# Performance work log

Hardware: AMD Instinct MI355X
Metric: run time of the kernel (lower is better)

## Reference

```python
import jax, jax.numpy as jnp
import numpy as np

NUM_HEADS = 16

def setup_inputs() -> dict:
    key = jax.random.key(0)
    k1, k2, k3 = jax.random.split(key, 3)
    B, N, C = 4, 4096, 1024
    x = jax.random.normal(k1, (B, N, C), dtype=jnp.float32)
    # xavier-uniform-ish scaled init for the dense kernels
    w_qkv = jax.random.normal(k2, (C, 3 * C), dtype=jnp.float32) * (2.0 / (C + 3 * C)) ** 0.5
    w_proj = jax.random.normal(k3, (C, C), dtype=jnp.float32) * (1.0 / C) ** 0.5
    b_proj = jnp.zeros((C,), dtype=jnp.float32)
    return {"x": x, "w_qkv": w_qkv, "w_proj": w_proj, "b_proj": b_proj}

def reference(x, w_qkv, w_proj, b_proj):
    B, N, C = x.shape
    H = NUM_HEADS
    D = C // H
    # qkv projection: (B, N, 3C) -> (3, B, H, N, D)
    qkv = (x @ w_qkv).reshape(B, N, 3, H, D).transpose(2, 0, 3, 1, 4)
    q, k, v = qkv[0], qkv[1], qkv[2]
    # feature map: elu + 1 (positive features)
    q = jax.nn.elu(q) + 1.0
    k = jax.nn.elu(k) + 1.0
    # kv outer-product accumulation: (B, H, D, D)
    kv = jnp.einsum('bhnd,bhne->bhde', k, v)
    numerator = jnp.einsum('bhnd,bhde->bhne', q, kv)        # (B, H, N, D)
    sum_k = k.sum(axis=-2)                                   # (B, H, D)
    denominator = jnp.einsum('bhnd,bhd->bhn', q, sum_k)[..., None]  # (B, H, N, 1)
    y = numerator / denominator                              # (B, H, N, D)
    y = y.transpose(0, 2, 1, 3).reshape(B, N, C)             # merge heads
    out = y @ w_proj + b_proj
    return out
```

## Files before the change

### kernel.cpp

```cpp
#include <hip/hip_runtime.h>

typedef __bf16 bf16x8 __attribute__((ext_vector_type(8)));
typedef float f32x4 __attribute__((ext_vector_type(4)));

typedef const unsigned int __attribute__((address_space(1)))* gas_p;
typedef unsigned int __attribute__((address_space(3)))* las_p;

__device__ __forceinline__ void gload_lds16(const void* g, void* l) {
  __builtin_amdgcn_global_load_lds((gas_p)g, (las_p)l, 16, 0, 0);
}

__device__ __forceinline__ unsigned short f2bf(float f) {
  union { float f; unsigned int u; } x; x.f = f;
  unsigned int r = x.u + 0x7fffu + ((x.u >> 16) & 1u);
  return (unsigned short)(r >> 16);
}
__device__ __forceinline__ float elu1(float x) {
  return x > 0.f ? x + 1.f : __expf(x);
}
__device__ __forceinline__ f32x4 mfma16(bf16x8 a, bf16x8 b, f32x4 c) {
  return __builtin_amdgcn_mfma_f32_16x16x32_bf16(a, b, c, 0, 0, 0);
}

#define BAR() __builtin_amdgcn_s_barrier()
#define VMW0() asm volatile("s_waitcnt vmcnt(0)" ::: "memory")


__global__ __launch_bounds__(256) void k_cvt_x(const float* __restrict__ x,
                                               unsigned short* __restrict__ xb, int n) {
  int i = (blockIdx.x * 256 + threadIdx.x) * 4;
  const int stride = gridDim.x * 256 * 4;
  for (; i < n; i += stride) {
    float4 v = *(const float4*)(x + i);
    union { unsigned short u[4]; uint2 q; } pk;
    pk.u[0] = f2bf(v.x); pk.u[1] = f2bf(v.y); pk.u[2] = f2bf(v.z); pk.u[3] = f2bf(v.w);
    *(uint2*)(xb + i) = pk.q;
  }
}

__global__ __launch_bounds__(256) void k_cvt_t(const float* __restrict__ w,
                                               unsigned short* __restrict__ wT,
                                               int R, int Cc) {
  __shared__ float t[32][33];
  const int j0 = blockIdx.x * 32, i0 = blockIdx.y * 32;
  const int tx = threadIdx.x & 31, ty = threadIdx.x >> 5;
#pragma unroll
  for (int k = 0; k < 4; ++k)
    t[ty + 8 * k][tx] = w[(size_t)(i0 + ty + 8 * k) * Cc + j0 + tx];
  __syncthreads();
#pragma unroll
  for (int k = 0; k < 4; ++k)
    wT[(size_t)(j0 + ty + 8 * k) * R + i0 + tx] = f2bf(t[tx][ty + 8 * k]);
}


template <int EPI>
__global__ __launch_bounds__(512, 2) void k_gemm256(
    const unsigned short* __restrict__ A, const unsigned short* __restrict__ BT, int NBX,
    unsigned short* __restrict__ qb, unsigned short* __restrict__ kT,
    unsigned short* __restrict__ vT, const float* __restrict__ bias,
    float* __restrict__ out) {
  extern __shared__ unsigned short lds[];
  unsigned short* Asb = lds;
  unsigned short* Bsb = lds + 32768;

  const int tid = threadIdx.x, lane = tid & 63, wave = tid >> 6;
  const int wm = wave >> 2, wn = wave & 3;
  int bid = blockIdx.x;
  { const int cpx = (int)gridDim.x >> 3; bid = (bid & 7) * cpx + (bid >> 3); }
  const int bx = bid % NBX, by = bid / NBX;
  const size_t bm0 = (size_t)by << 8, bn0 = (size_t)bx << 8;

  const int srow = (wave << 4) + (lane >> 2);
  const int gscol = ((lane & 3) << 3) ^ (((srow >> 1) & 3) << 3);
  const unsigned short* Ag0 = A + (bm0 + srow) * 1024 + gscol;
  const unsigned short* Bg0 = BT + (bn0 + srow) * 1024 + gscol;
  const int lws = wave << 9;

  auto stageA = [&](int pair) {
    const unsigned short* g_ = Ag0 + (pair << 5);
    unsigned short* l_ = Asb + ((pair & 3) << 13) + lws;
    gload_lds16(g_, l_);
    gload_lds16(g_ + 128 * 1024, l_ + 4096);
  };
  auto stageB = [&](int pair) {
    const unsigned short* g_ = Bg0 + (pair << 5);
    unsigned short* l_ = Bsb + ((pair & 3) << 13) + lws;
    gload_lds16(g_, l_);
    gload_lds16(g_ + 128 * 1024, l_ + 4096);
  };

  const int q8 = ((lane >> 4) << 3) ^ (((lane >> 1) & 3) << 3);
  const int ar_base = (wm << 7) + (lane & 15);
  const int br_base = (wn << 6) + (lane & 15);

  f32x4 acc[8][4] = {};

  stageA(0); stageB(0); stageA(1); stageB(1);
  VMW0();
  BAR();

#pragma unroll
  for (int t = 0; t < 16; ++t) {
    const int o0 = ((2 * t) & 3) << 13, o1 = ((2 * t + 1) & 3) << 13;

    if (t < 15) { stageA(2 * t + 2); stageB(2 * t + 2); stageA(2 * t + 3); stageB(2 * t + 3); }

    bf16x8 a0[4], a1[4], b0[4], b1[4];
#pragma unroll
    for (int mi = 0; mi < 4; ++mi)
      a0[mi] = *(const bf16x8*)&Asb[o0 + ((ar_base + mi * 16) << 5) + q8];
#pragma unroll
    for (int n = 0; n < 4; ++n)
      b0[n] = *(const bf16x8*)&Bsb[o0 + ((br_base + n * 16) << 5) + q8];
#pragma unroll
    for (int mi = 0; mi < 4; ++mi)
      a1[mi] = *(const bf16x8*)&Asb[o1 + ((ar_base + mi * 16) << 5) + q8];
#pragma unroll
    for (int n = 0; n < 4; ++n)
      b1[n] = *(const bf16x8*)&Bsb[o1 + ((br_base + n * 16) << 5) + q8];
    __builtin_amdgcn_s_setprio(1);
#pragma unroll
    for (int mi = 0; mi < 4; ++mi)
#pragma unroll
      for (int n = 0; n < 4; ++n) acc[mi][n] = mfma16(a0[mi], b0[n], acc[mi][n]);
#pragma unroll
    for (int mi = 0; mi < 4; ++mi)
#pragma unroll
      for (int n = 0; n < 4; ++n) acc[mi][n] = mfma16(a1[mi], b1[n], acc[mi][n]);
    __builtin_amdgcn_s_setprio(0);

#pragma unroll
    for (int mi = 0; mi < 4; ++mi)
      a0[mi] = *(const bf16x8*)&Asb[o0 + ((ar_base + 64 + mi * 16) << 5) + q8];
#pragma unroll
    for (int mi = 0; mi < 4; ++mi)
      a1[mi] = *(const bf16x8*)&Asb[o1 + ((ar_base + 64 + mi * 16) << 5) + q8];
    __builtin_amdgcn_s_setprio(1);
#pragma unroll
    for (int mi = 0; mi < 4; ++mi)
#pragma unroll
      for (int n = 0; n < 4; ++n) acc[4 + mi][n] = mfma16(a0[mi], b0[n], acc[4 + mi][n]);
#pragma unroll
    for (int mi = 0; mi < 4; ++mi)
#pragma unroll
      for (int n = 0; n < 4; ++n) acc[4 + mi][n] = mfma16(a1[mi], b1[n], acc[4 + mi][n]);
    __builtin_amdgcn_s_setprio(0);

    if (t < 15) VMW0();
    BAR();
  }

  const int rbase = (int)bm0 + (wm << 7) + ((lane >> 4) << 2);
  const int cbase = (int)bn0 + (wn << 6) + (lane & 15);
  if constexpr (EPI == 0) {
    const int reg3 = (int)(bn0 >> 10);
#pragma unroll
    for (int m = 0; m < 8; ++m) {
      const int rb = rbase + m * 16;
#pragma unroll
      for (int n = 0; n < 4; ++n) {
        const int col = cbase + n * 16;
        if (reg3 == 0) {
#pragma unroll
          for (int i = 0; i < 4; ++i)
            qb[(size_t)(rb + i) * 1024 + col] = f2bf(elu1(acc[m][n][i]));
        } else {
          const int jc = col & 1023, h = jc >> 6, d = jc & 63;
          const int b_ = rb >> 12, n_ = rb & 4095;
          union { unsigned short u[4]; uint2 q; } pk;
          if (reg3 == 1) {
#pragma unroll
            for (int i = 0; i < 4; ++i) pk.u[i] = f2bf(elu1(acc[m][n][i]));
          } else {
#pragma unroll
            for (int i = 0; i < 4; ++i) pk.u[i] = f2bf(acc[m][n][i]);
          }
          unsigned short* dst = (reg3 == 1) ? kT : vT;
          *(uint2*)(dst + ((size_t)((b_ * 16 + h) * 64 + d) * 4096 + n_)) = pk.q;
        }
      }
    }
  } else {
#pragma unroll
    for (int n = 0; n < 4; ++n) {
      const int col = cbase + n * 16;
      const float bc = bias[col];
#pragma unroll
      for (int m = 0; m < 8; ++m) {
        const int rb = rbase + m * 16;
#pragma unroll
        for (int i = 0; i < 4; ++i)
          out[(size_t)(rb + i) * 1024 + col] = acc[m][n][i] + bc;
      }
    }
  }
}


__global__ __launch_bounds__(256) void k_kvpart(const unsigned short* __restrict__ kT,
                                                const unsigned short* __restrict__ vT,
                                                float* __restrict__ kvp,
                                                float* __restrict__ sumkp) {
  __shared__ unsigned short Ks[64 * 64];
  __shared__ unsigned short Vs[64 * 64];
  const int blk = blockIdx.x;
  const int bh = blk >> 3, ch = blk & 7;
  const int tid = threadIdx.x, lane = tid & 63, wave = tid >> 6;
  const unsigned short* kb = kT + (size_t)bh * 64 * 4096;
  const unsigned short* vb = vT + (size_t)bh * 64 * 4096;
  const int n0 = ch * 512;
  const int lrow = lane >> 3;
  const int lcolz = (((lane & 7) ^ (lane >> 3)) << 3);
  f32x4 acc[5] = {};

  bf16x8 ones_frag;
  {
    unsigned short o = ((lane & 15) == 0) ? (unsigned short)0x3F80 : (unsigned short)0;
    union { unsigned short u[8]; bf16x8 v; } c;
#pragma unroll
    for (int i = 0; i < 8; ++i) c.u[i] = o;
    ones_frag = c.v;
  }

  const int rxor = (lane & 7) << 3;
  const int col0 = (((lane >> 4) << 3)) ^ rxor;
  const int col1 = ((32 + ((lane >> 4) << 3))) ^ rxor;

  for (int ks = 0; ks < 512; ks += 64) {
    __syncthreads();
#pragma unroll
    for (int i = 0; i < 2; ++i) {
      const int c = i * 4 + wave;
      gload_lds16(kb + (size_t)(c * 8 + lrow) * 4096 + n0 + ks + lcolz, &Ks[c * 512]);
      gload_lds16(vb + (size_t)(c * 8 + lrow) * 4096 + n0 + ks + lcolz, &Vs[c * 512]);
    }
    __syncthreads();
    const int ar = wave * 16 + (lane & 15);
#pragma unroll
    for (int kk = 0; kk < 2; ++kk) {
      const int co = kk ? col1 : col0;
      bf16x8 a = *(const bf16x8*)&Ks[ar * 64 + co];
#pragma unroll
      for (int n = 0; n < 4; ++n) {
        bf16x8 bv = *(const bf16x8*)&Vs[(n * 16 + (lane & 15)) * 64 + co];
        acc[n] = mfma16(a, bv, acc[n]);
      }
      acc[4] = mfma16(a, ones_frag, acc[4]);
    }
  }
  float* dst = kvp + (size_t)blk * 64 * 64;
  const int d0 = wave * 16 + ((lane >> 4) << 2);
#pragma unroll
  for (int n = 0; n < 4; ++n)
#pragma unroll
    for (int i = 0; i < 4; ++i)
      dst[(d0 + i) * 64 + n * 16 + (lane & 15)] = acc[n][i];
  if ((lane & 15) == 0) {
#pragma unroll
    for (int i = 0; i < 4; ++i) sumkp[(size_t)blk * 64 + d0 + i] = acc[4][i];
  }
}


__global__ __launch_bounds__(256) void k_kvred(const float* __restrict__ kvp,
                                               const float* __restrict__ sumkp,
                                               unsigned short* __restrict__ kvsk) {
  const int bh = blockIdx.x, tid = threadIdx.x;
  const float* src = kvp + (size_t)bh * 8 * 4096;
  unsigned short* dst = kvsk + (size_t)bh * 80 * 64;
#pragma unroll
  for (int it = 0; it < 16; ++it) {
    const int idx = tid + it * 256;
    const int e = idx >> 6, d = idx & 63;
    float s = 0.f;
#pragma unroll
    for (int c = 0; c < 8; ++c) s += src[c * 4096 + d * 64 + e];
    dst[idx] = f2bf(s);
  }
#pragma unroll
  for (int it = 0; it < 4; ++it) {
    const int idx = tid + it * 256;
    const int e2 = idx >> 6, d = idx & 63;
    float v = 0.f;
    if (e2 == 0) {
#pragma unroll
      for (int c = 0; c < 8; ++c) v += sumkp[(size_t)(bh * 8 + c) * 64 + d];
    }
    dst[64 * 64 + idx] = f2bf(v);
  }
}


__global__ __launch_bounds__(256) void k_numer(const unsigned short* __restrict__ qb,
                                               const unsigned short* __restrict__ kvsk,
                                               unsigned short* __restrict__ yb) {
  __shared__ unsigned short Bs[80 * 64];
  const int bh = blockIdx.y;
  const int b = bh >> 4, h = bh & 15;
  const int n0 = blockIdx.x << 7;
  const int tid = threadIdx.x, lane = tid & 63, wave = tid >> 6;
  {
    const uint4* src = (const uint4*)(kvsk + (size_t)bh * 80 * 64);
    uint4* dst = (uint4*)Bs;
    for (int i = tid; i < 640; i += 256) dst[i ^ ((i >> 3) & 7)] = src[i];
  }
  __syncthreads();

  const int ko = (lane >> 4) << 3;
  const int rx = (lane & 7) << 3;
  f32x4 acc[2][5] = {};
  const unsigned short* qrow =
      qb + (size_t)(b * 4096 + n0 + wave * 32 + (lane & 15)) * 1024 + h * 64;
#pragma unroll
  for (int kk = 0; kk < 2; ++kk) {
    bf16x8 a[2], bb[5];
#pragma unroll
    for (int m = 0; m < 2; ++m)
      a[m] = *(const bf16x8*)(qrow + (size_t)m * 16 * 1024 + ko + kk * 32);
#pragma unroll
    for (int n = 0; n < 5; ++n)
      bb[n] = *(const bf16x8*)&Bs[(n * 16 + (lane & 15)) * 64 + ((ko + kk * 32) ^ rx)];
#pragma unroll
    for (int m = 0; m < 2; ++m)
#pragma unroll
      for (int n = 0; n < 5; ++n)
        acc[m][n] = mfma16(a[m], bb[n], acc[m][n]);
  }

  const int rbase = b * 4096 + n0 + wave * 32 + ((lane >> 4) << 2);
#pragma unroll
  for (int m = 0; m < 2; ++m) {
    f32x4 inv;
#pragma unroll
    for (int i = 0; i < 4; ++i) {
      float den = __shfl(acc[m][4][i], lane & 48);
      inv[i] = __builtin_amdgcn_rcpf(den);
    }
#pragma unroll
    for (int n = 0; n < 4; ++n) {
      const int col = h * 64 + n * 16 + (lane & 15);
#pragma unroll
      for (int i = 0; i < 4; ++i)
        yb[(size_t)(rbase + m * 16 + i) * 1024 + col] = f2bf(acc[m][n][i] * inv[i]);
    }
  }
}


extern "C" void kernel_launch(void* const* d_in, const int* in_sizes, int n_in,
                              void* d_out, int out_size, void* d_ws, size_t ws_size,
                              hipStream_t stream) {
  const float* x = (const float*)d_in[0];
  const float* w_qkv = (const float*)d_in[1];
  const float* w_proj = (const float*)d_in[2];
  const float* b_proj = (const float*)d_in[3];
  float* out = (float*)d_out;
  char* ws = (char*)d_ws;

  unsigned short* xb = (unsigned short*)(ws);
  unsigned short* wqkvT = (unsigned short*)(ws + 33554432);
  unsigned short* wprojT = (unsigned short*)(ws + 39845888);
  unsigned short* qb = (unsigned short*)(ws + 41943040);
  unsigned short* kT = (unsigned short*)(ws + 75497472);
  unsigned short* vT = (unsigned short*)(ws + 109051904);
  float* kvp = (float*)(ws + 142606336);
  unsigned short* kvsk = (unsigned short*)(ws + 151011328);
  unsigned short* yb = xb;
  float* sumkp = (float*)wqkvT;

  k_cvt_x<<<2048, 256, 0, stream>>>(x, xb, 4 * 4096 * 1024);
  k_cvt_t<<<dim3(96, 32), 256, 0, stream>>>(w_qkv, wqkvT, 1024, 3072);
  k_cvt_t<<<dim3(32, 32), 256, 0, stream>>>(w_proj, wprojT, 1024, 1024);
  k_gemm256<0><<<768, 512, 131072, stream>>>(xb, wqkvT, 12, qb, kT, vT, nullptr, nullptr);
  k_kvpart<<<512, 256, 0, stream>>>(kT, vT, kvp, sumkp);
  k_kvred<<<64, 256, 0, stream>>>(kvp, sumkp, kvsk);
  k_numer<<<dim3(32, 64), 256, 0, stream>>>(qb, kvsk, yb);
  k_gemm256<1><<<256, 512, 131072, stream>>>(yb, wprojT, 4, nullptr, nullptr, nullptr,
                                             b_proj, out);
}
```

Before: 218.9 us.

## Software-pipeline LDS fragment reads with register double-buffering in QKV GEMM

Restructures the GEMM main loop so the fragments for the next k-slice are read from LDS into registers while MFMAs on the current slice run. Global prefetch now runs three slices ahead instead of two, using a partial vmcnt wait in the prologue. The goal is to hide LDS read latency behind MFMA work. In exchange, register pressure rises from holding two full A/B fragment sets, and the LDS slot reuse and wait ordering become more delicate.

```diff
diff --git a/kernel.cpp b/kernel.cpp
--- a/kernel.cpp
+++ b/kernel.cpp
@@ -23,7 +23,10 @@
 }
 
 #define BAR() __builtin_amdgcn_s_barrier()
+#define VMW8() asm volatile("s_waitcnt vmcnt(8)" ::: "memory")
 #define VMW0() asm volatile("s_waitcnt vmcnt(0)" ::: "memory")
+#define LGKM0() do { asm volatile("s_waitcnt lgkmcnt(0)" ::: "memory"); \
+                     __builtin_amdgcn_sched_barrier(0); } while (0)
 
 
 __global__ __launch_bounds__(256) void k_cvt_x(const float* __restrict__ x,
@@ -94,61 +97,66 @@
   const int ar_base = (wm << 7) + (lane & 15);
   const int br_base = (wn << 6) + (lane & 15);
 
+  auto rdA = [&](int slot, int m) {
+    return *(const bf16x8*)&Asb[(slot << 13) + ((ar_base + m * 16) << 5) + q8];
+  };
+  auto rdB = [&](int slot, int n) {
+    return *(const bf16x8*)&Bsb[(slot << 13) + ((br_base + n * 16) << 5) + q8];
+  };
+
   f32x4 acc[8][4] = {};
-
-  stageA(0); stageB(0); stageA(1); stageB(1);
+  bf16x8 fA0[8], fB0[4];
+
+  stageA(0); stageB(0);
+  stageA(1); stageB(1);
+  stageA(2); stageB(2);
+  VMW8();
+  BAR();
+#pragma unroll
+  for (int m = 0; m < 8; ++m) fA0[m] = rdA(0, m);
+#pragma unroll
+  for (int n = 0; n < 4; ++n) fB0[n] = rdB(0, n);
+  LGKM0();
   VMW0();
   BAR();
 
 #pragma unroll
   for (int t = 0; t < 16; ++t) {
-    const int o0 = ((2 * t) & 3) << 13, o1 = ((2 * t + 1) & 3) << 13;
-
-    if (t < 15) { stageA(2 * t + 2); stageB(2 * t + 2); stageA(2 * t + 3); stageB(2 * t + 3); }
-
-    bf16x8 a0[4], a1[4], b0[4], b1[4];
-#pragma unroll
-    for (int mi = 0; mi < 4; ++mi)
-      a0[mi] = *(const bf16x8*)&Asb[o0 + ((ar_base + mi * 16) << 5) + q8];
-#pragma unroll
-    for (int n = 0; n < 4; ++n)
-      b0[n] = *(const bf16x8*)&Bsb[o0 + ((br_base + n * 16) << 5) + q8];
-#pragma unroll
-    for (int mi = 0; mi < 4; ++mi)
-      a1[mi] = *(const bf16x8*)&Asb[o1 + ((ar_base + mi * 16) << 5) + q8];
-#pragma unroll
-    for (int n = 0; n < 4; ++n)
-      b1[n] = *(const bf16x8*)&Bsb[o1 + ((br_base + n * 16) << 5) + q8];
+    const int s1 = (2 * t + 1) & 3, s2 = (2 * t + 2) & 3;
+
+    if (t <= 14) { stageA(2 * t + 3); stageB(2 * t + 3); }
+    if (t <= 13) { stageA(2 * t + 4); stageB(2 * t + 4); }
+
+    bf16x8 fA1[8], fB1[4];
+#pragma unroll
+    for (int m = 0; m < 8; ++m) fA1[m] = rdA(s1, m);
+#pragma unroll
+    for (int n = 0; n < 4; ++n) fB1[n] = rdB(s1, n);
     __builtin_amdgcn_s_setprio(1);
 #pragma unroll
-    for (int mi = 0; mi < 4; ++mi)
-#pragma unroll
-      for (int n = 0; n < 4; ++n) acc[mi][n] = mfma16(a0[mi], b0[n], acc[mi][n]);
-#pragma unroll
-    for (int mi = 0; mi < 4; ++mi)
-#pragma unroll
-      for (int n = 0; n < 4; ++n) acc[mi][n] = mfma16(a1[mi], b1[n], acc[mi][n]);
+    for (int m = 0; m < 8; ++m)
+#pragma unroll
+      for (int n = 0; n < 4; ++n) acc[m][n] = mfma16(fA0[m], fB0[n], acc[m][n]);
     __builtin_amdgcn_s_setprio(0);
 
-#pragma unroll
-    for (int mi = 0; mi < 4; ++mi)
-      a0[mi] = *(const bf16x8*)&Asb[o0 + ((ar_base + 64 + mi * 16) << 5) + q8];
-#pragma unroll
-    for (int mi = 0; mi < 4; ++mi)
-      a1[mi] = *(const bf16x8*)&Asb[o1 + ((ar_base + 64 + mi * 16) << 5) + q8];
+    if (t <= 14) {
+#pragma unroll
+      for (int m = 0; m < 8; ++m) fA0[m] = rdA(s2, m);
+#pragma unroll
+      for (int n = 0; n < 4; ++n) fB0[n] = rdB(s2, n);
+    }
     __builtin_amdgcn_s_setprio(1);
 #pragma unroll
-    for (int mi = 0; mi < 4; ++mi)
-#pragma unroll
-      for (int n = 0; n < 4; ++n) acc[4 + mi][n] = mfma16(a0[mi], b0[n], acc[4 + mi][n]);
-#pragma unroll
-    for (int mi = 0; mi < 4; ++mi)
-#pragma unroll
-      for (int n = 0; n < 4; ++n) acc[4 + mi][n] = mfma16(a1[mi], b1[n], acc[4 + mi][n]);
+    for (int m = 0; m < 8; ++m)
+#pragma unroll
+      for (int n = 0; n < 4; ++n) acc[m][n] = mfma16(fA1[m], fB1[n], acc[m][n]);
     __builtin_amdgcn_s_setprio(0);
 
-    if (t < 15) VMW0();
-    BAR();
+    if (t <= 14) {
+      LGKM0();
+      VMW0();
+      BAR();
+    }
   }
 
   const int rbase = (int)bm0 + (wm << 7) + ((lane >> 4) << 2);
```

New measurement: 220.6 us. About the same (+0.8%).

## Deepen GEMM prefetch pipeline and double-buffer k_kvpart LDS staging

Applied to the files above, without the earlier changes.

The GEMM main loop now keeps three K-pairs in flight instead of two. Each iteration is split into four MFMA phases, and the loads for the next stage are interleaved between them using partial vmcnt waits and extra barriers, so global-to-LDS copies overlap with compute instead of draining to vmcnt(0) once per iteration. The kv partial kernel gains double-buffered K and V tiles in LDS, so the next chunk loads while the current one is multiplied. This adds more barriers and tighter ordering of the waits, and the kvpart kernel uses twice the LDS, which could hurt occupancy.

```diff
diff --git a/kernel.cpp b/kernel.cpp
--- a/kernel.cpp
+++ b/kernel.cpp
@@ -23,7 +23,10 @@
 }
 
 #define BAR() __builtin_amdgcn_s_barrier()
+#define VMW8() asm volatile("s_waitcnt vmcnt(8)" ::: "memory")
+#define VMW4() asm volatile("s_waitcnt vmcnt(4)" ::: "memory")
 #define VMW0() asm volatile("s_waitcnt vmcnt(0)" ::: "memory")
+#define LGKMW() asm volatile("s_waitcnt lgkmcnt(0)" ::: "memory")
 
 
 __global__ __launch_bounds__(256) void k_cvt_x(const float* __restrict__ x,
@@ -96,58 +99,78 @@
 
   f32x4 acc[8][4] = {};
 
-  stageA(0); stageB(0); stageA(1); stageB(1);
-  VMW0();
+  stageA(0); stageB(0);
+  stageA(1); stageB(1);
+  stageA(2); stageB(2);
+  VMW8();
   BAR();
 
 #pragma unroll
   for (int t = 0; t < 16; ++t) {
-    const int o0 = ((2 * t) & 3) << 13, o1 = ((2 * t + 1) & 3) << 13;
-
-    if (t < 15) { stageA(2 * t + 2); stageB(2 * t + 2); stageA(2 * t + 3); stageB(2 * t + 3); }
-
-    bf16x8 a0[4], a1[4], b0[4], b1[4];
-#pragma unroll
-    for (int mi = 0; mi < 4; ++mi)
-      a0[mi] = *(const bf16x8*)&Asb[o0 + ((ar_base + mi * 16) << 5) + q8];
+    const int s0 = ((2 * t) & 3) << 13, s1 = ((2 * t + 1) & 3) << 13;
+    bf16x8 fA[4], fB[4], gA[4];
+
+#pragma unroll
+    for (int mi = 0; mi < 4; ++mi)
+      fA[mi] = *(const bf16x8*)&Asb[s0 + ((ar_base + mi * 16) << 5) + q8];
 #pragma unroll
     for (int n = 0; n < 4; ++n)
-      b0[n] = *(const bf16x8*)&Bsb[o0 + ((br_base + n * 16) << 5) + q8];
-#pragma unroll
-    for (int mi = 0; mi < 4; ++mi)
-      a1[mi] = *(const bf16x8*)&Asb[o1 + ((ar_base + mi * 16) << 5) + q8];
+      fB[n] = *(const bf16x8*)&Bsb[s0 + ((br_base + n * 16) << 5) + q8];
+    if (t <= 14) stageA(2 * t + 3);
+    BAR();
+    LGKMW();
+    __builtin_amdgcn_s_setprio(1);
+#pragma unroll
+    for (int mi = 0; mi < 4; ++mi)
+#pragma unroll
+      for (int n = 0; n < 4; ++n) acc[mi][n] = mfma16(fA[mi], fB[n], acc[mi][n]);
+    __builtin_amdgcn_s_setprio(0);
+    BAR();
+
+#pragma unroll
+    for (int mi = 0; mi < 4; ++mi)
+      gA[mi] = *(const bf16x8*)&Asb[s0 + ((ar_base + 64 + mi * 16) << 5) + q8];
+    if (t <= 14) { stageB(2 * t + 3); VMW8(); } else { VMW0(); }
+    BAR();
+    LGKMW();
+    __builtin_amdgcn_s_setprio(1);
+#pragma unroll
+    for (int mi = 0; mi < 4; ++mi)
+#pragma unroll
+      for (int n = 0; n < 4; ++n) acc[4 + mi][n] = mfma16(gA[mi], fB[n], acc[4 + mi][n]);
+    __builtin_amdgcn_s_setprio(0);
+    BAR();
+
+#pragma unroll
+    for (int mi = 0; mi < 4; ++mi)
+      fA[mi] = *(const bf16x8*)&Asb[s1 + ((ar_base + mi * 16) << 5) + q8];
 #pragma unroll
     for (int n = 0; n < 4; ++n)
-      b1[n] = *(const bf16x8*)&Bsb[o1 + ((br_base + n * 16) << 5) + q8];
+      fB[n] = *(const bf16x8*)&Bsb[s1 + ((br_base + n * 16) << 5) + q8];
+    if (t <= 13) stageA(2 * t + 4);
+    BAR();
+    LGKMW();
     __builtin_amdgcn_s_setprio(1);
 #pragma unroll
     for (int mi = 0; mi < 4; ++mi)
 #pragma unroll
-      for (int n = 0; n < 4; ++n) acc[mi][n] = mfma16(a0[mi], b0[n], acc[mi][n]);
-#pragma unroll
-    for (int mi = 0; mi < 4; ++mi)
-#pragma unroll
-      for (int n = 0; n < 4; ++n) acc[mi][n] = mfma16(a1[mi], b1[n], acc[mi][n]);
+      for (int n = 0; n < 4; ++n) acc[mi][n] = mfma16(fA[mi], fB[n], acc[mi][n]);
     __builtin_amdgcn_s_setprio(0);
-
-#pragma unroll
-    for (int mi = 0; mi < 4; ++mi)
-      a0[mi] = *(const bf16x8*)&Asb[o0 + ((ar_base + 64 + mi * 16) << 5) + q8];
-#pragma unroll
-    for (int mi = 0; mi < 4; ++mi)
-      a1[mi] = *(const bf16x8*)&Asb[o1 + ((ar_base + 64 + mi * 16) << 5) + q8];
+    BAR();
+
+#pragma unroll
+    for (int mi = 0; mi < 4; ++mi)
+      gA[mi] = *(const bf16x8*)&Asb[s1 + ((ar_base + 64 + mi * 16) << 5) + q8];
+    if (t <= 13) { stageB(2 * t + 4); VMW8(); }
+    else if (t == 14) { VMW4(); }
+    BAR();
+    LGKMW();
     __builtin_amdgcn_s_setprio(1);
 #pragma unroll
     for (int mi = 0; mi < 4; ++mi)
 #pragma unroll
-      for (int n = 0; n < 4; ++n) acc[4 + mi][n] = mfma16(a0[mi], b0[n], acc[4 + mi][n]);
-#pragma unroll
-    for (int mi = 0; mi < 4; ++mi)
-#pragma unroll
-      for (int n = 0; n < 4; ++n) acc[4 + mi][n] = mfma16(a1[mi], b1[n], acc[4 + mi][n]);
+      for (int n = 0; n < 4; ++n) acc[4 + mi][n] = mfma16(gA[mi], fB[n], acc[4 + mi][n]);
     __builtin_amdgcn_s_setprio(0);
-
-    if (t < 15) VMW0();
     BAR();
   }
 
@@ -202,8 +225,8 @@
                                                 const unsigned short* __restrict__ vT,
                                                 float* __restrict__ kvp,
                                                 float* __restrict__ sumkp) {
-  __shared__ unsigned short Ks[64 * 64];
-  __shared__ unsigned short Vs[64 * 64];
+  __shared__ unsigned short Ks[2][64 * 64];
+  __shared__ unsigned short Vs[2][64 * 64];
   const int blk = blockIdx.x;
   const int bh = blk >> 3, ch = blk & 7;
   const int tid = threadIdx.x, lane = tid & 63, wave = tid >> 6;
@@ -214,6 +237,15 @@
   const int lcolz = (((lane & 7) ^ (lane >> 3)) << 3);
   f32x4 acc[5] = {};
 
+  auto stage = [&](int buf, int ks) {
+#pragma unroll
+    for (int i = 0; i < 2; ++i) {
+      const int c = i * 4 + wave;
+      gload_lds16(kb + (size_t)(c * 8 + lrow) * 4096 + n0 + ks + lcolz, &Ks[buf][c * 512]);
+      gload_lds16(vb + (size_t)(c * 8 + lrow) * 4096 + n0 + ks + lcolz, &Vs[buf][c * 512]);
+    }
+  };
+
   bf16x8 ones_frag;
   {
     unsigned short o = ((lane & 15) == 0) ? (unsigned short)0x3F80 : (unsigned short)0;
@@ -227,28 +259,30 @@
   const int col0 = (((lane >> 4) << 3)) ^ rxor;
   const int col1 = ((32 + ((lane >> 4) << 3))) ^ rxor;
 
-  for (int ks = 0; ks < 512; ks += 64) {
-    __syncthreads();
-#pragma unroll
-    for (int i = 0; i < 2; ++i) {
-      const int c = i * 4 + wave;
-      gload_lds16(kb + (size_t)(c * 8 + lrow) * 4096 + n0 + ks + lcolz, &Ks[c * 512]);
-      gload_lds16(vb + (size_t)(c * 8 + lrow) * 4096 + n0 + ks + lcolz, &Vs[c * 512]);
-    }
-    __syncthreads();
+  stage(0, 0);
+  VMW0();
+  BAR();
+
+#pragma unroll
+  for (int it = 0; it < 8; ++it) {
+    const int buf = it & 1;
+    if (it < 7) stage(buf ^ 1, (it + 1) * 64);
     const int ar = wave * 16 + (lane & 15);
 #pragma unroll
     for (int kk = 0; kk < 2; ++kk) {
       const int co = kk ? col1 : col0;
-      bf16x8 a = *(const bf16x8*)&Ks[ar * 64 + co];
+      bf16x8 a = *(const bf16x8*)&Ks[buf][ar * 64 + co];
 #pragma unroll
       for (int n = 0; n < 4; ++n) {
-        bf16x8 bv = *(const bf16x8*)&Vs[(n * 16 + (lane & 15)) * 64 + co];
+        bf16x8 bv = *(const bf16x8*)&Vs[buf][(n * 16 + (lane & 15)) * 64 + co];
         acc[n] = mfma16(a, bv, acc[n]);
       }
       acc[4] = mfma16(a, ones_frag, acc[4]);
     }
-  }
+    if (it < 7) { VMW0(); }
+    BAR();
+  }
+
   float* dst = kvp + (size_t)blk * 64 * 64;
   const int d0 = wave * 16 + ((lane >> 4) << 2);
 #pragma unroll
```

Result: no change. 221.1 us (+1.0%).

## Replace pipelined 256x256 GEMM with simple 128x128 single-buffered GEMM and merge weight transposes

Applied to the files above, without the earlier changes.

Swaps the 256x256-tile, 512-thread, four-stage LDS-pipelined GEMM for a 128x128-tile, 256-thread kernel that loads one 32-wide K slice per iteration with barriers on both sides, so there is no overlap of loads and MFMA. It also merges the two weight transpose/convert launches into one kernel. The smaller tiles give more blocks and less LDS per block, but double global traffic per FLOP and serialize memory latency with compute.

```diff
diff --git a/kernel.cpp b/kernel.cpp
--- a/kernel.cpp
+++ b/kernel.cpp
@@ -38,11 +38,16 @@
   }
 }
 
-__global__ __launch_bounds__(256) void k_cvt_t(const float* __restrict__ w,
-                                               unsigned short* __restrict__ wT,
-                                               int R, int Cc) {
+__global__ __launch_bounds__(256) void k_cvt_t2(const float* __restrict__ wq,
+                                                unsigned short* __restrict__ wqT,
+                                                const float* __restrict__ wp,
+                                                unsigned short* __restrict__ wpT) {
   __shared__ float t[32][33];
-  const int j0 = blockIdx.x * 32, i0 = blockIdx.y * 32;
+  const int bx = blockIdx.x;
+  const float* w = (bx < 96) ? wq : wp;
+  unsigned short* wT = (bx < 96) ? wqT : wpT;
+  const int Cc = (bx < 96) ? 3072 : 1024;
+  const int j0 = ((bx < 96) ? bx : bx - 96) * 32, i0 = blockIdx.y * 32;
   const int tx = threadIdx.x & 31, ty = threadIdx.x >> 5;
 #pragma unroll
   for (int k = 0; k < 4; ++k)
@@ -50,113 +55,68 @@
   __syncthreads();
 #pragma unroll
   for (int k = 0; k < 4; ++k)
-    wT[(size_t)(j0 + ty + 8 * k) * R + i0 + tx] = f2bf(t[tx][ty + 8 * k]);
+    wT[(size_t)(j0 + ty + 8 * k) * 1024 + i0 + tx] = f2bf(t[tx][ty + 8 * k]);
 }
 
 
 template <int EPI>
-__global__ __launch_bounds__(512, 2) void k_gemm256(
+__global__ __launch_bounds__(256, 3) void k_gemm128(
     const unsigned short* __restrict__ A, const unsigned short* __restrict__ BT, int NBX,
     unsigned short* __restrict__ qb, unsigned short* __restrict__ kT,
     unsigned short* __restrict__ vT, const float* __restrict__ bias,
     float* __restrict__ out) {
-  extern __shared__ unsigned short lds[];
-  unsigned short* Asb = lds;
-  unsigned short* Bsb = lds + 32768;
+  __shared__ unsigned short Asb[128 * 32];
+  __shared__ unsigned short Bsb[128 * 32];
 
   const int tid = threadIdx.x, lane = tid & 63, wave = tid >> 6;
-  const int wm = wave >> 2, wn = wave & 3;
+  const int wm = wave >> 1, wn = wave & 1;
   int bid = blockIdx.x;
   { const int cpx = (int)gridDim.x >> 3; bid = (bid & 7) * cpx + (bid >> 3); }
   const int bx = bid % NBX, by = bid / NBX;
-  const size_t bm0 = (size_t)by << 8, bn0 = (size_t)bx << 8;
+  const size_t bm0 = (size_t)by << 7, bn0 = (size_t)bx << 7;
 
   const int srow = (wave << 4) + (lane >> 2);
-  const int gscol = ((lane & 3) << 3) ^ (((srow >> 1) & 3) << 3);
-  const unsigned short* Ag0 = A + (bm0 + srow) * 1024 + gscol;
-  const unsigned short* Bg0 = BT + (bn0 + srow) * 1024 + gscol;
-  const int lws = wave << 9;
-
-  auto stageA = [&](int pair) {
-    const unsigned short* g_ = Ag0 + (pair << 5);
-    unsigned short* l_ = Asb + ((pair & 3) << 13) + lws;
-    gload_lds16(g_, l_);
-    gload_lds16(g_ + 128 * 1024, l_ + 4096);
-  };
-  auto stageB = [&](int pair) {
-    const unsigned short* g_ = Bg0 + (pair << 5);
-    unsigned short* l_ = Bsb + ((pair & 3) << 13) + lws;
-    gload_lds16(g_, l_);
-    gload_lds16(g_ + 128 * 1024, l_ + 4096);
-  };
-
-  const int q8 = ((lane >> 4) << 3) ^ (((lane >> 1) & 3) << 3);
-  const int ar_base = (wm << 7) + (lane & 15);
-  const int br_base = (wn << 6) + (lane & 15);
-
-  f32x4 acc[8][4] = {};
-
-  stageA(0); stageB(0); stageA(1); stageB(1);
-  VMW0();
-  BAR();
-
-#pragma unroll
-  for (int t = 0; t < 16; ++t) {
-    const int o0 = ((2 * t) & 3) << 13, o1 = ((2 * t + 1) & 3) << 13;
-
-    if (t < 15) { stageA(2 * t + 2); stageB(2 * t + 2); stageA(2 * t + 3); stageB(2 * t + 3); }
-
-    bf16x8 a0[4], a1[4], b0[4], b1[4];
-#pragma unroll
-    for (int mi = 0; mi < 4; ++mi)
-      a0[mi] = *(const bf16x8*)&Asb[o0 + ((ar_base + mi * 16) << 5) + q8];
+  const int scol = (((lane & 3) ^ ((lane >> 2) & 3)) << 3);
+  const unsigned short* Ag = A + (bm0 + srow) * 1024 + scol;
+  const unsigned short* Bg = BT + (bn0 + srow) * 1024 + scol;
+  unsigned short* Al = Asb + (wave << 9) + (lane << 3);
+  unsigned short* Bl = Bsb + (wave << 9) + (lane << 3);
+
+  const int qsw = (((lane >> 4) ^ (lane & 3)) << 3);
+  const int arow = (wm << 6) + (lane & 15);
+  const int brow = (wn << 6) + (lane & 15);
+
+  f32x4 acc[4][4] = {};
+
+  for (int ks = 0; ks < 1024; ks += 32) {
+    BAR();
+    gload_lds16(Ag + ks, Al);
+    gload_lds16(Ag + 64 * 1024 + ks, Al + 2048);
+    gload_lds16(Bg + ks, Bl);
+    gload_lds16(Bg + 64 * 1024 + ks, Bl + 2048);
+    VMW0();
+    BAR();
+    bf16x8 a[4], b[4];
+#pragma unroll
+    for (int m = 0; m < 4; ++m)
+      a[m] = *(const bf16x8*)&Asb[((arow + m * 16) << 5) + qsw];
 #pragma unroll
     for (int n = 0; n < 4; ++n)
-      b0[n] = *(const bf16x8*)&Bsb[o0 + ((br_base + n * 16) << 5) + q8];
-#pragma unroll
-    for (int mi = 0; mi < 4; ++mi)
-      a1[mi] = *(const bf16x8*)&Asb[o1 + ((ar_base + mi * 16) << 5) + q8];
-#pragma unroll
-    for (int n = 0; n < 4; ++n)
-      b1[n] = *(const bf16x8*)&Bsb[o1 + ((br_base + n * 16) << 5) + q8];
+      b[n] = *(const bf16x8*)&Bsb[((brow + n * 16) << 5) + qsw];
     __builtin_amdgcn_s_setprio(1);
 #pragma unroll
-    for (int mi = 0; mi < 4; ++mi)
-#pragma unroll
-      for (int n = 0; n < 4; ++n) acc[mi][n] = mfma16(a0[mi], b0[n], acc[mi][n]);
-#pragma unroll
-    for (int mi = 0; mi < 4; ++mi)
-#pragma unroll
-      for (int n = 0; n < 4; ++n) acc[mi][n] = mfma16(a1[mi], b1[n], acc[mi][n]);
+    for (int m = 0; m < 4; ++m)
+#pragma unroll
+      for (int n = 0; n < 4; ++n) acc[m][n] = mfma16(a[m], b[n], acc[m][n]);
     __builtin_amdgcn_s_setprio(0);
-
-#pragma unroll
-    for (int mi = 0; mi < 4; ++mi)
-      a0[mi] = *(const bf16x8*)&Asb[o0 + ((ar_base + 64 + mi * 16) << 5) + q8];
-#pragma unroll
-    for (int mi = 0; mi < 4; ++mi)
-      a1[mi] = *(const bf16x8*)&Asb[o1 + ((ar_base + 64 + mi * 16) << 5) + q8];
-    __builtin_amdgcn_s_setprio(1);
-#pragma unroll
-    for (int mi = 0; mi < 4; ++mi)
-#pragma unroll
-      for (int n = 0; n < 4; ++n) acc[4 + mi][n] = mfma16(a0[mi], b0[n], acc[4 + mi][n]);
-#pragma unroll
-    for (int mi = 0; mi < 4; ++mi)
-#pragma unroll
-      for (int n = 0; n < 4; ++n) acc[4 + mi][n] = mfma16(a1[mi], b1[n], acc[4 + mi][n]);
-    __builtin_amdgcn_s_setprio(0);
-
-    if (t < 15) VMW0();
-    BAR();
-  }
-
-  const int rbase = (int)bm0 + (wm << 7) + ((lane >> 4) << 2);
+  }
+
+  const int rbase = (int)bm0 + (wm << 6) + ((lane >> 4) << 2);
   const int cbase = (int)bn0 + (wn << 6) + (lane & 15);
   if constexpr (EPI == 0) {
     const int reg3 = (int)(bn0 >> 10);
 #pragma unroll
-    for (int m = 0; m < 8; ++m) {
+    for (int m = 0; m < 4; ++m) {
       const int rb = rbase + m * 16;
 #pragma unroll
       for (int n = 0; n < 4; ++n) {
@@ -187,7 +147,7 @@
       const int col = cbase + n * 16;
       const float bc = bias[col];
 #pragma unroll
-      for (int m = 0; m < 8; ++m) {
+      for (int m = 0; m < 4; ++m) {
         const int rb = rbase + m * 16;
 #pragma unroll
         for (int i = 0; i < 4; ++i)
@@ -370,12 +330,11 @@
   float* sumkp = (float*)wqkvT;
 
   k_cvt_x<<<2048, 256, 0, stream>>>(x, xb, 4 * 4096 * 1024);
-  k_cvt_t<<<dim3(96, 32), 256, 0, stream>>>(w_qkv, wqkvT, 1024, 3072);
-  k_cvt_t<<<dim3(32, 32), 256, 0, stream>>>(w_proj, wprojT, 1024, 1024);
-  k_gemm256<0><<<768, 512, 131072, stream>>>(xb, wqkvT, 12, qb, kT, vT, nullptr, nullptr);
+  k_cvt_t2<<<dim3(128, 32), 256, 0, stream>>>(w_qkv, wqkvT, w_proj, wprojT);
+  k_gemm128<0><<<3072, 256, 0, stream>>>(xb, wqkvT, 24, qb, kT, vT, nullptr, nullptr);
   k_kvpart<<<512, 256, 0, stream>>>(kT, vT, kvp, sumkp);
   k_kvred<<<64, 256, 0, stream>>>(kvp, sumkp, kvsk);
   k_numer<<<dim3(32, 64), 256, 0, stream>>>(qb, kvsk, yb);
-  k_gemm256<1><<<256, 512, 131072, stream>>>(yb, wprojT, 4, nullptr, nullptr, nullptr,
-                                             b_proj, out);
-}
+  k_gemm128<1><<<1024, 256, 0, stream>>>(yb, wprojT, 8, nullptr, nullptr, nullptr,
+                                         b_proj, out);
+}
```

Result: slower. 241.5 us (+10.3%).
